# Optimization experiments

Hardware: AMD Instinct MI355X
Metric: run time of the kernel (lower is better)

The kernel has to match this reference:

```python
import jax, jax.numpy as jnp
import numpy as np

B, AT, NBR = 8, 96, 512
NG, NT = 25, 5            # n_gaussian_triple, n_theta
NANG = NG * NT            # 125, filternet input dim
NF = 128                  # n_filters
NB = 128                  # n_atom_basis


def ssp(x):
    # shifted softplus: ln(0.5*e^x + 0.5) = softplus(x) - ln(2)
    return jax.nn.softplus(x) - jnp.asarray(np.log(2.0), x.dtype)


def setup_inputs() -> dict:
    key = jax.random.key(0)
    ks = jax.random.split(key, 16)
    s = lambda fan_in: 1.0 / np.sqrt(fan_in)
    return {
        "x": jax.random.normal(ks[0], (B, AT, NB), jnp.float32),
        "triple_ijk": jax.random.uniform(ks[1], (B, AT, NBR, NANG), jnp.float32),
        "neighbors_j": jax.random.randint(ks[2], (B, AT, NBR), 0, AT, jnp.int32),
        "neighbors_k": jax.random.randint(ks[3], (B, AT, NBR), 0, AT, jnp.int32),
        "triple_mask": jnp.ones((B, AT, NBR), jnp.float32),
        # filter network (Dense ssp -> Dense linear)
        "W1": jax.random.normal(ks[4], (NANG, NF), jnp.float32) * s(NANG),
        "b1": jnp.zeros((NF,), jnp.float32),
        "W2": jax.random.normal(ks[5], (NF, NF), jnp.float32) * s(NF),
        "b2": jnp.zeros((NF,), jnp.float32),
        # cfconv in2f (no bias) and f2out (ssp activation)
        "Win": jax.random.normal(ks[6], (NB, NF), jnp.float32) * s(NB),
        "Wf2": jax.random.normal(ks[7], (NF, NB), jnp.float32) * s(NF),
        "bf2": jnp.zeros((NB,), jnp.float32),
        # final dense (linear) before residual
        "Wd": jax.random.normal(ks[8], (NB, NB), jnp.float32) * s(NB),
        "bd": jnp.zeros((NB,), jnp.float32),
    }


def _gather_atoms(y, nbh):
    # y: (B, At, F); nbh: (B, At, Nbr) -> (B, At, Nbr, F)
    b, at, nbr = nbh.shape
    idx = nbh.reshape(b, at * nbr, 1)
    return jnp.take_along_axis(y, idx, axis=1).reshape(b, at, nbr, y.shape[-1])


def reference(x, triple_ijk, neighbors_j, neighbors_k, triple_mask,
              W1, b1, W2, b2, Win, Wf2, bf2, Wd, bd):
    # filter network on angular/radial triple features -> (B, At, Nbr, NF)
    W_triple = ssp(triple_ijk @ W1 + b1) @ W2 + b2
    # in2f
    y = x @ Win                                  # (B, At, NF)
    y_j = _gather_atoms(y, neighbors_j)          # (B, At, Nbr, NF)
    y_k = _gather_atoms(y, neighbors_k)          # (B, At, Nbr, NF)
    # element-wise continuous-filter conv over triples, mask padded triples
    yt = y_j * y_k * W_triple * triple_mask[..., None]
    agg = jnp.sum(yt, axis=2)                    # sum-aggregate over triples
    v = ssp(agg @ Wf2 + bf2)                     # f2out with shifted softplus
    v = v @ Wd + bd                              # interaction dense
    return x + v                                 # residual
```

## Files before the change

kernel.cpp:

```cpp
#include <hip/hip_runtime.h>
#include <math.h>

#define B_    8
#define AT_   96
#define NBR_  512
#define NANG_ 125
#define NF_   128
#define NB_   128
#define TN    32
#define NCHUNK 2
#define CROWS (NBR_ / NCHUNK)
#define NTI   (CROWS / TN)
#define TSTRIDE 136
#define YSTRIDE 36

typedef __attribute__((ext_vector_type(8))) short bf16x8;
typedef __attribute__((ext_vector_type(4))) float f32x4;

#define AS_G __attribute__((address_space(1)))
#define AS_L __attribute__((address_space(3)))

__device__ __forceinline__ short f2bf(float f) {
    union { float f; unsigned u; } x; x.f = f;
    return (short)((x.u + 0x8000u) >> 16);
}

__device__ __forceinline__ float sspf(float x) {
    float p = __builtin_amdgcn_exp2f(x * 1.44269504088896340736f);
    float l = __builtin_amdgcn_logf(1.0f + p);
    return 0.69314718055994530942f * l - 0.69314718055994530942f;
}

__device__ __forceinline__ bf16x8 cvt8(f32x4 lo, f32x4 hi) {
    unsigned r0, r1, r2, r3;
    asm("v_cvt_pk_bf16_f32 %0, %1, %2" : "=v"(r0) : "v"(lo.x), "v"(lo.y));
    asm("v_cvt_pk_bf16_f32 %0, %1, %2" : "=v"(r1) : "v"(lo.z), "v"(lo.w));
    asm("v_cvt_pk_bf16_f32 %0, %1, %2" : "=v"(r2) : "v"(hi.x), "v"(hi.y));
    asm("v_cvt_pk_bf16_f32 %0, %1, %2" : "=v"(r3) : "v"(hi.z), "v"(hi.w));
    typedef __attribute__((ext_vector_type(4))) unsigned u32x4;
    u32x4 r = { r0, r1, r2, r3 };
    return __builtin_bit_cast(bf16x8, r);
}

__device__ __forceinline__ void gl_lds16(const void* g, void* l) {
    __builtin_amdgcn_global_load_lds((const AS_G void*)g, (AS_L void*)l, 16, 0, 0);
}

__device__ __forceinline__ void stage_tile(const float* g, float* l, int tid) {
    int wave = tid >> 6;
    const char* gb = (const char*)g + tid * 16;
    char* lb = (char*)l + wave * 1024;
    gl_lds16(gb,          lb);
    gl_lds16(gb + 4096,   lb + 4096);
    gl_lds16(gb + 8192,   lb + 8192);
    if (tid < 232)
        gl_lds16(gb + 12288, lb + 12288);
}

__global__ __launch_bounds__(128) void prep_kernel(
    const float* __restrict__ x, const float* __restrict__ Win,
    const float* __restrict__ W1, const float* __restrict__ W2,
    float* __restrict__ y, short* __restrict__ w1p, short* __restrict__ w2p)
{
    __shared__ float xs[4][NB_];
    int blk = blockIdx.x, tid = threadIdx.x;
    if (blk < 192) {
        int row0 = blk * 4;
        #pragma unroll
        for (int r = 0; r < 4; r++) xs[r][tid] = x[(row0 + r) * NB_ + tid];
        __syncthreads();
        float a0 = 0.f, a1 = 0.f, a2 = 0.f, a3 = 0.f;
        #pragma unroll 8
        for (int k = 0; k < NB_; k++) {
            float w = Win[k * NF_ + tid];
            a0 = fmaf(xs[0][k], w, a0);
            a1 = fmaf(xs[1][k], w, a1);
            a2 = fmaf(xs[2][k], w, a2);
            a3 = fmaf(xs[3][k], w, a3);
        }
        y[(row0 + 0) * NF_ + tid] = a0;
        y[(row0 + 1) * NF_ + tid] = a1;
        y[(row0 + 2) * NF_ + tid] = a2;
        y[(row0 + 3) * NF_ + tid] = a3;
    } else {
        int t = (blk - 192) * 128 + tid;
        int j = t & 7, lane = (t >> 3) & 63, ks = (t >> 9) & 3, ct = t >> 11;
        int k = ks * 32 + (lane >> 4) * 8 + j;
        int n = ct * 16 + (lane & 15);
        w1p[t] = (k < NANG_) ? f2bf(W1[k * NF_ + n]) : (short)0;
        w2p[t] = f2bf(W2[k * NF_ + n]);
    }
}

__global__ __launch_bounds__(256) void triple_partial(
    const float* __restrict__ trip,
    const int* __restrict__ nbj, const int* __restrict__ nbk,
    const float* __restrict__ maskg,
    const float* __restrict__ b1g, const float* __restrict__ b2g,
    const float* __restrict__ y, const short* __restrict__ w1p,
    const short* __restrict__ w2p, float* __restrict__ pagg)
{
    __shared__ float ldsT[2][4008];
    __shared__ short hs[2][TN * TSTRIDE];
    __shared__ float yjkw[4][TN * YSTRIDE];

    const int tid = threadIdx.x;
    const int wave = tid >> 6, lane = tid & 63;
    const int quad = lane >> 4, col = lane & 15;
    const int blk = blockIdx.x;
    const int bid = blk >> 1, c = blk & 1;
    const int b = bid / AT_;

    const float* tpc = trip + (long)bid * NBR_ * NANG_ + (long)c * CROWS * NANG_;
    const int nb_base = bid * NBR_ + c * CROWS;

    const int ct0 = 2 * wave, ct1 = 2 * wave + 1;
    const int f0 = ct0 * 16 + col, f1 = ct1 * 16 + col;
    const float bias1_0 = b1g[f0], bias1_1 = b1g[f1];
    const float bias2_0 = b2g[f0], bias2_1 = b2g[f1];

    const int row2 = lane >> 1, h = lane & 1;
    const int ycol = wave * 32 + h * 16;

    bf16x8 w1f0[4], w1f1[4], w2f0[4], w2f1[4];
    #pragma unroll
    for (int ks = 0; ks < 4; ks++) {
        w1f0[ks] = *(const bf16x8*)&w1p[(ct0 * 4 + ks) * 512 + lane * 8];
        w1f1[ks] = *(const bf16x8*)&w1p[(ct1 * 4 + ks) * 512 + lane * 8];
        w2f0[ks] = *(const bf16x8*)&w2p[(ct0 * 4 + ks) * 512 + lane * 8];
        w2f1[ks] = *(const bf16x8*)&w2p[(ct1 * 4 + ks) * 512 + lane * 8];
    }

    if (tid < 8) { ldsT[0][4000 + tid] = 0.f; ldsT[1][4000 + tid] = 0.f; }

    stage_tile(tpc, &ldsT[0][0], tid);
    int jj = nbj[nb_base + row2];
    int kk = nbk[nb_base + row2];
    float mk = maskg[nb_base + row2];

    __syncthreads();

    float accw0 = 0.f, accw1 = 0.f;
    int cur = 0;

    for (int nt = 0; nt < NTI; nt++) {
        if (nt + 1 < NTI)
            stage_tile(tpc + (nt + 1) * (TN * NANG_), &ldsT[cur ^ 1][0], tid);

        const float* yj = y + (b * AT_ + jj) * NF_ + ycol;
        const float* yk = y + (b * AT_ + kk) * NF_ + ycol;
        f32x4 j0 = ((const f32x4*)yj)[0], j1 = ((const f32x4*)yj)[1];
        f32x4 j2 = ((const f32x4*)yj)[2], j3 = ((const f32x4*)yj)[3];
        f32x4 k0 = ((const f32x4*)yk)[0], k1 = ((const f32x4*)yk)[1];
        f32x4 k2 = ((const f32x4*)yk)[2], k3 = ((const f32x4*)yk)[3];
        const float mc = mk;
        if (nt + 1 < NTI) {
            jj = nbj[nb_base + (nt + 1) * TN + row2];
            kk = nbk[nb_base + (nt + 1) * TN + row2];
            mk = maskg[nb_base + (nt + 1) * TN + row2];
        }

        const float* rA = &ldsT[cur][col * NANG_];
        const float* rB = &ldsT[cur][(16 + col) * NANG_];
        f32x4 d00 = {0,0,0,0}, d01 = {0,0,0,0}, d10 = {0,0,0,0}, d11 = {0,0,0,0};
        #pragma unroll
        for (int ks = 0; ks < 4; ks++) {
            const int ko = ks * 32 + quad * 8;
            float a[8], bfl[8];
            #pragma unroll
            for (int j = 0; j < 8; j++) a[j] = rA[ko + j];
            #pragma unroll
            for (int j = 0; j < 8; j++) bfl[j] = rB[ko + j];
            bf16x8 a0 = cvt8((f32x4){a[0],a[1],a[2],a[3]}, (f32x4){a[4],a[5],a[6],a[7]});
            bf16x8 a1 = cvt8((f32x4){bfl[0],bfl[1],bfl[2],bfl[3]}, (f32x4){bfl[4],bfl[5],bfl[6],bfl[7]});
            d00 = __builtin_amdgcn_mfma_f32_16x16x32_bf16(a0, w1f0[ks], d00, 0, 0, 0);
            d01 = __builtin_amdgcn_mfma_f32_16x16x32_bf16(a0, w1f1[ks], d01, 0, 0, 0);
            d10 = __builtin_amdgcn_mfma_f32_16x16x32_bf16(a1, w1f0[ks], d10, 0, 0, 0);
            d11 = __builtin_amdgcn_mfma_f32_16x16x32_bf16(a1, w1f1[ks], d11, 0, 0, 0);
        }

        {
            float* d = &yjkw[wave][row2 * YSTRIDE + h * 16];
            *(f32x4*)(d + 0)  = j0 * k0 * mc;
            *(f32x4*)(d + 4)  = j1 * k1 * mc;
            *(f32x4*)(d + 8)  = j2 * k2 * mc;
            *(f32x4*)(d + 12) = j3 * k3 * mc;
        }
        #pragma unroll
        for (int r = 0; r < 4; r++) {
            int row0 = quad * 4 + r, row1 = 16 + quad * 4 + r;
            hs[cur][row0 * TSTRIDE + f0] = f2bf(sspf(d00[r] + bias1_0));
            hs[cur][row0 * TSTRIDE + f1] = f2bf(sspf(d01[r] + bias1_1));
            hs[cur][row1 * TSTRIDE + f0] = f2bf(sspf(d10[r] + bias1_0));
            hs[cur][row1 * TSTRIDE + f1] = f2bf(sspf(d11[r] + bias1_1));
        }
        __syncthreads();

        f32x4 e00 = {0,0,0,0}, e01 = {0,0,0,0}, e10 = {0,0,0,0}, e11 = {0,0,0,0};
        #pragma unroll
        for (int ks = 0; ks < 4; ks++) {
            bf16x8 a0 = *(const bf16x8*)&hs[cur][(     col) * TSTRIDE + ks * 32 + quad * 8];
            bf16x8 a1 = *(const bf16x8*)&hs[cur][(16 + col) * TSTRIDE + ks * 32 + quad * 8];
            e00 = __builtin_amdgcn_mfma_f32_16x16x32_bf16(a0, w2f0[ks], e00, 0, 0, 0);
            e01 = __builtin_amdgcn_mfma_f32_16x16x32_bf16(a0, w2f1[ks], e01, 0, 0, 0);
            e10 = __builtin_amdgcn_mfma_f32_16x16x32_bf16(a1, w2f0[ks], e10, 0, 0, 0);
            e11 = __builtin_amdgcn_mfma_f32_16x16x32_bf16(a1, w2f1[ks], e11, 0, 0, 0);
        }
        const float* yw = &yjkw[wave][0];
        #pragma unroll
        for (int r = 0; r < 4; r++) {
            int row0 = quad * 4 + r, row1 = 16 + quad * 4 + r;
            accw0 += (e00[r] + bias2_0) * yw[row0 * YSTRIDE + col];
            accw1 += (e01[r] + bias2_1) * yw[row0 * YSTRIDE + col + 16];
            accw0 += (e10[r] + bias2_0) * yw[row1 * YSTRIDE + col];
            accw1 += (e11[r] + bias2_1) * yw[row1 * YSTRIDE + col + 16];
        }
        cur ^= 1;
    }

    accw0 += __shfl_xor(accw0, 16, 64);
    accw0 += __shfl_xor(accw0, 32, 64);
    accw1 += __shfl_xor(accw1, 16, 64);
    accw1 += __shfl_xor(accw1, 32, 64);
    if (quad == 0) {
        pagg[blk * NF_ + f0] = accw0;
        pagg[blk * NF_ + f1] = accw1;
    }
}

__global__ __launch_bounds__(128) void finish_kernel(
    const float* __restrict__ x, const float* __restrict__ pagg,
    const float* __restrict__ Wf2, const float* __restrict__ bf2,
    const float* __restrict__ Wd, const float* __restrict__ bd,
    float* __restrict__ out)
{
    __shared__ float aggs[NF_];
    __shared__ float t1s[NF_];
    int bid = blockIdx.x, f = threadIdx.x;
    float a = pagg[(bid * 2 + 0) * NF_ + f] + pagg[(bid * 2 + 1) * NF_ + f];
    aggs[f] = a;
    __syncthreads();
    float acc = 0.f;
    #pragma unroll 8
    for (int k = 0; k < NF_; k++) acc = fmaf(aggs[k], Wf2[k * NB_ + f], acc);
    t1s[f] = sspf(acc + bf2[f]);
    __syncthreads();
    acc = 0.f;
    #pragma unroll 8
    for (int k = 0; k < NB_; k++) acc = fmaf(t1s[k], Wd[k * NB_ + f], acc);
    out[bid * NB_ + f] = x[bid * NB_ + f] + acc + bd[f];
}

extern "C" void kernel_launch(void* const* d_in, const int* in_sizes, int n_in,
                              void* d_out, int out_size, void* d_ws, size_t ws_size,
                              hipStream_t stream) {
    const float* x    = (const float*)d_in[0];
    const float* trip = (const float*)d_in[1];
    const int*   nbj  = (const int*)d_in[2];
    const int*   nbk  = (const int*)d_in[3];
    const float* mask = (const float*)d_in[4];
    const float* W1   = (const float*)d_in[5];
    const float* b1   = (const float*)d_in[6];
    const float* W2   = (const float*)d_in[7];
    const float* b2   = (const float*)d_in[8];
    const float* Win  = (const float*)d_in[9];
    const float* Wf2  = (const float*)d_in[10];
    const float* bf2  = (const float*)d_in[11];
    const float* Wd   = (const float*)d_in[12];
    const float* bd   = (const float*)d_in[13];
    float* out = (float*)d_out;

    char* ws = (char*)d_ws;
    float* y    = (float*)ws;
    short* w1p  = (short*)(ws + 393216);
    short* w2p  = (short*)(ws + 393216 + 32768);
    float* pagg = (float*)(ws + 393216 + 65536);

    prep_kernel<<<320, 128, 0, stream>>>(x, Win, W1, W2, y, w1p, w2p);
    triple_partial<<<B_ * AT_ * NCHUNK, 256, 0, stream>>>(trip, nbj, nbk, mask,
        b1, b2, y, w1p, w2p, pagg);
    finish_kernel<<<B_ * AT_, 128, 0, stream>>>(x, pagg, Wf2, bf2, Wd, bd, out);
}
```

Measured before the change: 347.2 us.

## Stage triple tiles as bf16 in registers with XOR-swizzled LDS layout

```diff
diff --git a/kernel.cpp b/kernel.cpp
--- a/kernel.cpp
+++ b/kernel.cpp
@@ -11,14 +11,11 @@
 #define NCHUNK 2
 #define CROWS (NBR_ / NCHUNK)
 #define NTI   (CROWS / TN)
-#define TSTRIDE 136
 #define YSTRIDE 36
 
 typedef __attribute__((ext_vector_type(8))) short bf16x8;
 typedef __attribute__((ext_vector_type(4))) float f32x4;
-
-#define AS_G __attribute__((address_space(1)))
-#define AS_L __attribute__((address_space(3)))
+typedef __attribute__((ext_vector_type(4))) unsigned u32x4;
 
 __device__ __forceinline__ short f2bf(float f) {
     union { float f; unsigned u; } x; x.f = f;
@@ -31,30 +28,31 @@
     return 0.69314718055994530942f * l - 0.69314718055994530942f;
 }
 
-__device__ __forceinline__ bf16x8 cvt8(f32x4 lo, f32x4 hi) {
-    unsigned r0, r1, r2, r3;
-    asm("v_cvt_pk_bf16_f32 %0, %1, %2" : "=v"(r0) : "v"(lo.x), "v"(lo.y));
-    asm("v_cvt_pk_bf16_f32 %0, %1, %2" : "=v"(r1) : "v"(lo.z), "v"(lo.w));
-    asm("v_cvt_pk_bf16_f32 %0, %1, %2" : "=v"(r2) : "v"(hi.x), "v"(hi.y));
-    asm("v_cvt_pk_bf16_f32 %0, %1, %2" : "=v"(r3) : "v"(hi.z), "v"(hi.w));
-    typedef __attribute__((ext_vector_type(4))) unsigned u32x4;
-    u32x4 r = { r0, r1, r2, r3 };
-    return __builtin_bit_cast(bf16x8, r);
-}
-
-__device__ __forceinline__ void gl_lds16(const void* g, void* l) {
-    __builtin_amdgcn_global_load_lds((const AS_G void*)g, (AS_L void*)l, 16, 0, 0);
-}
-
-__device__ __forceinline__ void stage_tile(const float* g, float* l, int tid) {
-    int wave = tid >> 6;
-    const char* gb = (const char*)g + tid * 16;
-    char* lb = (char*)l + wave * 1024;
-    gl_lds16(gb,          lb);
-    gl_lds16(gb + 4096,   lb + 4096);
-    gl_lds16(gb + 8192,   lb + 8192);
-    if (tid < 232)
-        gl_lds16(gb + 12288, lb + 12288);
+__device__ __forceinline__ void load_tile(const float* __restrict__ tile,
+                                          int row, int seg, float* v) {
+    const float* s = tile + row * NANG_ + seg * 16;
+    if (seg < 7) {
+        #pragma unroll
+        for (int j = 0; j < 16; j++) v[j] = s[j];
+    } else {
+        #pragma unroll
+        for (int j = 0; j < 13; j++) v[j] = s[j];
+        v[13] = 0.f; v[14] = 0.f; v[15] = 0.f;
+    }
+}
+
+__device__ __forceinline__ void store_tile(short* dst, int row, int seg, const float* v) {
+    unsigned r[8];
+    #pragma unroll
+    for (int i = 0; i < 8; i++) {
+        unsigned x;
+        asm("v_cvt_pk_bf16_f32 %0, %1, %2" : "=v"(x) : "v"(v[2 * i]), "v"(v[2 * i + 1]));
+        r[i] = x;
+    }
+    const int swz = (row & 7) << 4;
+    char* base = (char*)dst + row * 256;
+    *(u32x4*)(base + ((seg * 32) ^ swz))      = (u32x4){r[0], r[1], r[2], r[3]};
+    *(u32x4*)(base + ((seg * 32 + 16) ^ swz)) = (u32x4){r[4], r[5], r[6], r[7]};
 }
 
 __global__ __launch_bounds__(128) void prep_kernel(
@@ -92,7 +90,7 @@
     }
 }
 
-__global__ __launch_bounds__(256) void triple_partial(
+__global__ __launch_bounds__(256, 3) void triple_partial(
     const float* __restrict__ trip,
     const int* __restrict__ nbj, const int* __restrict__ nbk,
     const float* __restrict__ maskg,
@@ -100,8 +98,8 @@
     const float* __restrict__ y, const short* __restrict__ w1p,
     const short* __restrict__ w2p, float* __restrict__ pagg)
 {
-    __shared__ float ldsT[2][4008];
-    __shared__ short hs[2][TN * TSTRIDE];
+    __shared__ short tileT[2][TN * 128];
+    __shared__ short hs[2][TN * 128];
     __shared__ float yjkw[4][TN * YSTRIDE];
 
     const int tid = threadIdx.x;
@@ -119,8 +117,11 @@
     const float bias1_0 = b1g[f0], bias1_1 = b1g[f1];
     const float bias2_0 = b2g[f0], bias2_1 = b2g[f1];
 
+    const int trow = tid >> 3, tseg = tid & 7;
     const int row2 = lane >> 1, h = lane & 1;
     const int ycol = wave * 32 + h * 16;
+    const int swzA = (col & 7) << 4;
+    const int quad16 = quad * 16;
 
     bf16x8 w1f0[4], w1f1[4], w2f0[4], w2f1[4];
     #pragma unroll
@@ -131,13 +132,12 @@
         w2f1[ks] = *(const bf16x8*)&w2p[(ct1 * 4 + ks) * 512 + lane * 8];
     }
 
-    if (tid < 8) { ldsT[0][4000 + tid] = 0.f; ldsT[1][4000 + tid] = 0.f; }
-
-    stage_tile(tpc, &ldsT[0][0], tid);
+    float v[16];
+    load_tile(tpc, trow, tseg, v);
     int jj = nbj[nb_base + row2];
     int kk = nbk[nb_base + row2];
     float mk = maskg[nb_base + row2];
-
+    store_tile(&tileT[0][0], trow, tseg, v);
     __syncthreads();
 
     float accw0 = 0.f, accw1 = 0.f;
@@ -145,7 +145,7 @@
 
     for (int nt = 0; nt < NTI; nt++) {
         if (nt + 1 < NTI)
-            stage_tile(tpc + (nt + 1) * (TN * NANG_), &ldsT[cur ^ 1][0], tid);
+            load_tile(tpc + (nt + 1) * (TN * NANG_), trow, tseg, v);
 
         const float* yj = y + (b * AT_ + jj) * NF_ + ycol;
         const float* yk = y + (b * AT_ + kk) * NF_ + ycol;
@@ -160,19 +160,14 @@
             mk = maskg[nb_base + (nt + 1) * TN + row2];
         }
 
-        const float* rA = &ldsT[cur][col * NANG_];
-        const float* rB = &ldsT[cur][(16 + col) * NANG_];
+        const char* tbA = (const char*)&tileT[cur][0] + col * 256;
+        const char* tbB = (const char*)&tileT[cur][0] + (16 + col) * 256;
         f32x4 d00 = {0,0,0,0}, d01 = {0,0,0,0}, d10 = {0,0,0,0}, d11 = {0,0,0,0};
         #pragma unroll
         for (int ks = 0; ks < 4; ks++) {
-            const int ko = ks * 32 + quad * 8;
-            float a[8], bfl[8];
-            #pragma unroll
-            for (int j = 0; j < 8; j++) a[j] = rA[ko + j];
-            #pragma unroll
-            for (int j = 0; j < 8; j++) bfl[j] = rB[ko + j];
-            bf16x8 a0 = cvt8((f32x4){a[0],a[1],a[2],a[3]}, (f32x4){a[4],a[5],a[6],a[7]});
-            bf16x8 a1 = cvt8((f32x4){bfl[0],bfl[1],bfl[2],bfl[3]}, (f32x4){bfl[4],bfl[5],bfl[6],bfl[7]});
+            const int off = (ks * 64 + quad16) ^ swzA;
+            bf16x8 a0 = *(const bf16x8*)(tbA + off);
+            bf16x8 a1 = *(const bf16x8*)(tbB + off);
             d00 = __builtin_amdgcn_mfma_f32_16x16x32_bf16(a0, w1f0[ks], d00, 0, 0, 0);
             d01 = __builtin_amdgcn_mfma_f32_16x16x32_bf16(a0, w1f1[ks], d01, 0, 0, 0);
             d10 = __builtin_amdgcn_mfma_f32_16x16x32_bf16(a1, w1f0[ks], d10, 0, 0, 0);
@@ -186,21 +181,31 @@
             *(f32x4*)(d + 8)  = j2 * k2 * mc;
             *(f32x4*)(d + 12) = j3 * k3 * mc;
         }
-        #pragma unroll
-        for (int r = 0; r < 4; r++) {
-            int row0 = quad * 4 + r, row1 = 16 + quad * 4 + r;
-            hs[cur][row0 * TSTRIDE + f0] = f2bf(sspf(d00[r] + bias1_0));
-            hs[cur][row0 * TSTRIDE + f1] = f2bf(sspf(d01[r] + bias1_1));
-            hs[cur][row1 * TSTRIDE + f0] = f2bf(sspf(d10[r] + bias1_0));
-            hs[cur][row1 * TSTRIDE + f1] = f2bf(sspf(d11[r] + bias1_1));
-        }
+        {
+            char* hw = (char*)&hs[cur][0];
+            #pragma unroll
+            for (int r = 0; r < 4; r++) {
+                int row0 = quad * 4 + r, row1 = row0 + 16;
+                int s0 = (row0 & 7) << 4;
+                *(short*)(hw + row0 * 256 + ((2 * f0) ^ s0)) = f2bf(sspf(d00[r] + bias1_0));
+                *(short*)(hw + row0 * 256 + ((2 * f1) ^ s0)) = f2bf(sspf(d01[r] + bias1_1));
+                *(short*)(hw + row1 * 256 + ((2 * f0) ^ s0)) = f2bf(sspf(d10[r] + bias1_0));
+                *(short*)(hw + row1 * 256 + ((2 * f1) ^ s0)) = f2bf(sspf(d11[r] + bias1_1));
+            }
+        }
+        if (nt + 1 < NTI)
+            store_tile(&tileT[cur ^ 1][0], trow, tseg, v);
+
         __syncthreads();
 
+        const char* hbA = (const char*)&hs[cur][0] + col * 256;
+        const char* hbB = (const char*)&hs[cur][0] + (16 + col) * 256;
         f32x4 e00 = {0,0,0,0}, e01 = {0,0,0,0}, e10 = {0,0,0,0}, e11 = {0,0,0,0};
         #pragma unroll
         for (int ks = 0; ks < 4; ks++) {
-            bf16x8 a0 = *(const bf16x8*)&hs[cur][(     col) * TSTRIDE + ks * 32 + quad * 8];
-            bf16x8 a1 = *(const bf16x8*)&hs[cur][(16 + col) * TSTRIDE + ks * 32 + quad * 8];
+            const int off = (ks * 64 + quad16) ^ swzA;
+            bf16x8 a0 = *(const bf16x8*)(hbA + off);
+            bf16x8 a1 = *(const bf16x8*)(hbB + off);
             e00 = __builtin_amdgcn_mfma_f32_16x16x32_bf16(a0, w2f0[ks], e00, 0, 0, 0);
             e01 = __builtin_amdgcn_mfma_f32_16x16x32_bf16(a0, w2f1[ks], e01, 0, 0, 0);
             e10 = __builtin_amdgcn_mfma_f32_16x16x32_bf16(a1, w2f0[ks], e10, 0, 0, 0);
@@ -209,7 +214,7 @@
         const float* yw = &yjkw[wave][0];
         #pragma unroll
         for (int r = 0; r < 4; r++) {
-            int row0 = quad * 4 + r, row1 = 16 + quad * 4 + r;
+            int row0 = quad * 4 + r, row1 = row0 + 16;
             accw0 += (e00[r] + bias2_0) * yw[row0 * YSTRIDE + col];
             accw1 += (e01[r] + bias2_1) * yw[row0 * YSTRIDE + col + 16];
             accw0 += (e10[r] + bias2_0) * yw[row1 * YSTRIDE + col];
```

Measured after the change: 352.1 us. No clear change (+1.4%).
